# Kernel tuning notes

Hardware: AMD Instinct MI355X
Metric: run time of the kernel (lower is better)

Reference implementation:

```python
import jax, jax.numpy as jnp
import numpy as np


def _offdiag_cols(B):
    # cols[i, k] = k-th column index != i, ascending (matches masked_select on ~eye)
    r = jnp.arange(B - 1)[None, :]
    i = jnp.arange(B)[:, None]
    return jnp.where(r < i, r, r + 1)  # [B, B-1]


def _process_case(lan_s, vis, B):
    # lan_s: [B, D], vis: [B, V, D]
    lan_adj = lan_s @ lan_s.T                               # [B, B]
    # sim[b, a, v] = lan_s[b] . vis[a, v]  (torch 'avd,bqd->baqv' with q=1)
    sim = jnp.einsum('avd,bd->bav', vis, lan_s)             # [B, B, V]
    vals, idxs = jax.lax.top_k(sim, 2)                      # [B, B, 2]
    ar = jnp.arange(B)
    diag_idx = idxs[ar, ar, 0]                              # best region per matched pair
    selected = vis[ar, diag_idx]                            # [B, D]
    img_adj = selected @ selected.T                         # [B, B]
    # Slogits [B,B,1,1] -> max over trailing dims == plain matmul
    logits = selected @ lan_s.T                             # [B, B]

    max0 = vals[..., 0]                                     # [B, B]
    max1 = vals[..., 1]                                     # [B, B]
    cols = _offdiag_cols(B)
    max1_off = jnp.take_along_axis(max1, cols, axis=1)      # [B, B-1]
    new_logits = jnp.concatenate([max0, max1_off], axis=1)  # [B, 2B-1]
    # CrossEntropyLoss(mean) with target = arange(B)
    ce = -jnp.mean(jax.nn.log_softmax(new_logits, axis=1)[ar, ar])

    # Regularization pair loss on row-softmaxed max0; neg idx for sample i = all j != i,
    # duplicated (t2i and i2t are identical here) -> duplication cancels in the mean.
    score = jax.nn.softmax(max0, axis=1)                    # [B, B]
    d = jnp.diag(score)                                     # s_ii
    offmask = (1.0 - jnp.eye(B, dtype=score.dtype))
    denom = jnp.asarray(B * (B - 1), score.dtype)
    # t1[i,j] = |(s_ii - s_ji) - (s_jj - s_ij)|, t2[i,j] = |(s_ii - s_ij) - (s_jj - s_ji)|
    t1 = jnp.abs(d[:, None] - score.T - d[None, :] + score)
    t2 = jnp.abs(d[:, None] - score - d[None, :] + score.T)
    m1 = jnp.sum(t1 * offmask) / denom
    m2 = jnp.sum(t2 * offmask) / denom
    pairloss = jax.nn.relu(m1) + jax.nn.relu(m2)            # (L1 - margin).clamp(0), margin=0

    # L1 between adjacency softmax and logits softmax
    loss_fns = jnp.mean(jnp.abs(
        jax.nn.softmax((img_adj + lan_adj) * 0.5, axis=1) -
        jax.nn.softmax(logits, axis=1)))

    alpha = jnp.asarray(0.1, score.dtype)
    beta = jnp.asarray(0.1, score.dtype)
    return ce + alpha * loss_fns + beta * pairloss


def reference(vis_fs, lan_fs):
    B = vis_fs.shape[0]
    losses = [_process_case(lan_fs[:, i, :], vis_fs, B) for i in range(3)]
    return (losses[0] + losses[1] + losses[2]) / 3.0


def setup_inputs() -> dict:
    key = jax.random.key(0)
    k1, k2 = jax.random.split(key)
    B, V, D = 128, 784, 512
    # scale ~0.05 so dot products of D=512-dim embeddings stay in a sane softmax range
    vis_fs = jax.random.normal(k1, (B, V, D), dtype=jnp.float32) * 0.05
    lan_fs = jax.random.normal(k2, (B, 3, D), dtype=jnp.float32) * 0.05
    return {"vis_fs": vis_fs, "lan_fs": lan_fs}
```

## Files before the change

### kernel.cpp

```cpp
#include <hip/hip_runtime.h>
#include <math.h>

#define B_   128
#define V_   784
#define D_   512
#define M_   384
#define NCH  7
#define LO_OFF 196608

typedef __attribute__((ext_vector_type(8))) short short8;
typedef __attribute__((ext_vector_type(4))) float f32x4;

__device__ __forceinline__ ushort f2bf(float x) {
  uint u = __float_as_uint(x);
  u += 0x7fff + ((u >> 16) & 1);
  return (ushort)(u >> 16);
}
__device__ __forceinline__ float bf2f(ushort h) {
  return __uint_as_float((uint)h << 16);
}

__device__ __forceinline__ int swz(int row, int col) {
  return (row * 64 + col) ^ ((row & 7) << 3);
}

__device__ __forceinline__ short8 ldfrag(const ushort* base, int row, int col) {
  union { uint4 u; short8 s; } t;
  t.u = *(const uint4*)(base + swz(row, col));
  return t.s;
}

__global__ __launch_bounds__(256)
void prep_lan(const float* __restrict__ lan, ushort* __restrict__ lanbf,
              float* __restrict__ acc) {
  const int c = blockIdx.x, kb = blockIdx.y, t = threadIdx.x;
  if (c == 0 && kb == 0 && t < 12) acc[t] = 0.f;
  #pragma unroll
  for (int i = 0; i < 4; i++) {
    const int u = t + 256 * i;
    const int kk = u >> 9;
    const int m16 = (u >> 6) & 7;
    const int lane = u & 63;
    const int row = m16 * 16 + (lane & 15);
    const int k0 = kb * 64 + kk * 32 + (lane >> 4) * 8;
    const float4 v0 = *(const float4*)(lan + (size_t)(row * 3 + c) * D_ + k0);
    const float4 v1 = *(const float4*)(lan + (size_t)(row * 3 + c) * D_ + k0 + 4);
    union { ushort s[8]; uint4 u4; } h, l;
    const float vv[8] = {v0.x, v0.y, v0.z, v0.w, v1.x, v1.y, v1.z, v1.w};
    #pragma unroll
    for (int e = 0; e < 8; e++) {
      h.s[e] = f2bf(vv[e]);
      l.s[e] = f2bf(vv[e] - bf2f(h.s[e]));
    }
    const size_t ch = ((((size_t)(c * 8 + kb) * 2 + kk) * 8 + m16) * 64 + lane);
    *(uint4*)&lanbf[ch * 8] = h.u4;
    *(uint4*)&lanbf[LO_OFF + ch * 8] = l.u4;
  }
}

__global__ __launch_bounds__(512)
void gemm_top2(const float* __restrict__ vis, const ushort* __restrict__ lanbf,
               float* __restrict__ pv1, float* __restrict__ pv2,
               int* __restrict__ pi1) {
  const int id = blockIdx.x;
  const int a = id / NCH;
  const int nch = id - NCH * a;

  const int t = threadIdx.x;
  const int lane = t & 63, wid = t >> 6;
  const int tx = lane & 15, qq = lane >> 4;
  const int wr = wid >> 2, wc = wid & 3;

  __shared__ __align__(16) ushort Bsm[2][16384];

  f32x4 acc[3][4][2];
  const f32x4 zz = {0.f, 0.f, 0.f, 0.f};
  #pragma unroll
  for (int c = 0; c < 3; c++)
    #pragma unroll
    for (int m = 0; m < 4; m++)
      #pragma unroll
      for (int n = 0; n < 2; n++) acc[c][m][n] = zz;

  const int v0 = nch * 128;
  const float* visA = vis + (size_t)a * V_ * D_;

  float4 breg[4];
  #pragma unroll
  for (int i = 0; i < 4; i++) {
    const int f = t + 512 * i;
    const int row = f >> 4, col = (f & 15) * 4;
    const int vrow = v0 + row;
    breg[i] = (vrow < V_)
        ? *(const float4*)(visA + (size_t)vrow * D_ + col)
        : make_float4(0.f, 0.f, 0.f, 0.f);
  }
  #pragma unroll
  for (int i = 0; i < 4; i++) {
    const int f = t + 512 * i;
    const int row = f >> 4, col = (f & 15) * 4;
    const float4 v = breg[i];
    ushort4 h, l;
    h.x = f2bf(v.x); l.x = f2bf(v.x - bf2f(h.x));
    h.y = f2bf(v.y); l.y = f2bf(v.y - bf2f(h.y));
    h.z = f2bf(v.z); l.z = f2bf(v.z - bf2f(h.z));
    h.w = f2bf(v.w); l.w = f2bf(v.w - bf2f(h.w));
    const int e = swz(row, col);
    *(ushort4*)&Bsm[0][e] = h;
    *(ushort4*)&Bsm[0][8192 + e] = l;
  }
  __syncthreads();

  for (int kb = 0; kb < 8; kb++) {
    const int cur = kb & 1;
    if (kb < 7) {
      #pragma unroll
      for (int i = 0; i < 4; i++) {
        const int f = t + 512 * i;
        const int row = f >> 4, col = (f & 15) * 4;
        const int vrow = v0 + row;
        breg[i] = (vrow < V_)
            ? *(const float4*)(visA + (size_t)vrow * D_ + (kb + 1) * 64 + col)
            : make_float4(0.f, 0.f, 0.f, 0.f);
      }
    }
    const ushort* Bcur = &Bsm[cur][0];
    #pragma unroll
    for (int kk = 0; kk < 2; kk++) {
      short8 bh[2], bl[2];
      #pragma unroll
      for (int n = 0; n < 2; n++) {
        const int brow = 32 * wc + 16 * n + tx;
        const int bcol = kk * 32 + qq * 8;
        bh[n] = ldfrag(Bcur, brow, bcol);
        bl[n] = ldfrag(Bcur + 8192, brow, bcol);
      }
      #pragma unroll
      for (int c = 0; c < 3; c++) {
        const size_t ch0 =
            (((size_t)(c * 8 + kb) * 2 + kk) * 8 + wr * 4) * 64 + lane;
        short8 ah[4], al[4];
        #pragma unroll
        for (int m = 0; m < 4; m++) {
          ah[m] = *(const short8*)(lanbf + (ch0 + m * 64) * 8);
          al[m] = *(const short8*)(lanbf + (size_t)LO_OFF + (ch0 + m * 64) * 8);
        }
        #pragma unroll
        for (int m = 0; m < 4; m++)
          #pragma unroll
          for (int n = 0; n < 2; n++) {
            acc[c][m][n] = __builtin_amdgcn_mfma_f32_16x16x32_bf16(
                ah[m], bh[n], acc[c][m][n], 0, 0, 0);
            acc[c][m][n] = __builtin_amdgcn_mfma_f32_16x16x32_bf16(
                ah[m], bl[n], acc[c][m][n], 0, 0, 0);
            acc[c][m][n] = __builtin_amdgcn_mfma_f32_16x16x32_bf16(
                al[m], bh[n], acc[c][m][n], 0, 0, 0);
          }
      }
    }
    if (kb < 7) {
      #pragma unroll
      for (int i = 0; i < 4; i++) {
        const int f = t + 512 * i;
        const int row = f >> 4, col = (f & 15) * 4;
        const float4 v = breg[i];
        ushort4 h, l;
        h.x = f2bf(v.x); l.x = f2bf(v.x - bf2f(h.x));
        h.y = f2bf(v.y); l.y = f2bf(v.y - bf2f(h.y));
        h.z = f2bf(v.z); l.z = f2bf(v.z - bf2f(h.z));
        h.w = f2bf(v.w); l.w = f2bf(v.w - bf2f(h.w));
        const int e = swz(row, col);
        *(ushort4*)&Bsm[cur ^ 1][e] = h;
        *(ushort4*)&Bsm[cur ^ 1][8192 + e] = l;
      }
    }
    __syncthreads();
  }

  float* p1b = (float*)&Bsm[0][0];
  float* p2b = p1b + 512;
  int*   i1b = (int*)(p2b + 512);
  #pragma unroll
  for (int c = 0; c < 3; c++) {
    #pragma unroll
    for (int m = 0; m < 4; m++)
      #pragma unroll
      for (int r = 0; r < 4; r++) {
        float v1 = -INFINITY, v2 = -INFINITY;
        int i1 = 0x7fffffff;
        #pragma unroll
        for (int n = 0; n < 2; n++) {
          const int vv = v0 + 32 * wc + 16 * n + tx;
          const float x = acc[c][m][n][r];
          if (vv < V_) {
            if (x > v1) { v2 = v1; v1 = x; i1 = vv; }
            else if (x > v2) { v2 = x; }
          }
        }
        #pragma unroll
        for (int off = 8; off >= 1; off >>= 1) {
          const float ov1 = __shfl_xor(v1, off, 16);
          const float ov2 = __shfl_xor(v2, off, 16);
          const int   oi1 = __shfl_xor(i1, off, 16);
          if (ov1 > v1 || (ov1 == v1 && oi1 < i1)) {
            v2 = fmaxf(v1, ov2); v1 = ov1; i1 = oi1;
          } else {
            v2 = fmaxf(v2, ov1);
          }
        }
        if (tx == 0) {
          const int grow = 64 * wr + 16 * m + 4 * qq + r;
          p1b[wc * 128 + grow] = v1;
          p2b[wc * 128 + grow] = v2;
          i1b[wc * 128 + grow] = i1;
        }
      }
    __syncthreads();
    if (t < 128) {
      float v1 = p1b[t], v2 = p2b[t];
      int i1 = i1b[t];
      #pragma unroll
      for (int w = 1; w < 4; w++) {
        const float ov1 = p1b[w * 128 + t], ov2 = p2b[w * 128 + t];
        const int oi1 = i1b[w * 128 + t];
        if (ov1 > v1) { v2 = fmaxf(v1, ov2); v1 = ov1; i1 = oi1; }
        else          { v2 = fmaxf(v2, ov1); }
      }
      const size_t o = ((size_t)a * NCH + nch) * M_ + c * B_ + t;
      pv1[o] = v1; pv2[o] = v2; pi1[o] = i1;
    }
    __syncthreads();
  }
}

__global__ void reduce_top2(const float* __restrict__ pv1,
                            const float* __restrict__ pv2,
                            const int* __restrict__ pi1,
                            float* __restrict__ max0, float* __restrict__ max1,
                            int* __restrict__ didx) {
  const int idx = blockIdx.x * 256 + threadIdx.x;
  if (idx >= M_ * B_) return;
  const int m = idx >> 7, a = idx & 127;
  float v1 = -INFINITY, v2 = -INFINITY;
  int i1 = 0x7fffffff;
  #pragma unroll
  for (int nc = 0; nc < NCH; nc++) {
    const size_t o = ((size_t)a * NCH + nc) * M_ + m;
    const float ov1 = pv1[o], ov2 = pv2[o];
    const int oi1 = pi1[o];
    if (ov1 > v1 || (ov1 == v1 && oi1 < i1)) {
      v2 = fmaxf(v1, ov2); v1 = ov1; i1 = oi1;
    } else {
      v2 = fmaxf(v2, ov1);
    }
  }
  max0[idx] = v1;
  max1[idx] = v2;
  const int b = m & 127, cc = m >> 7;
  if (b == a) didx[(cc << 7) + b] = i1;
}

__global__ void gather_sel(const float* __restrict__ vis,
                           const int* __restrict__ didx,
                           float* __restrict__ sel) {
  const int cb = blockIdx.x;
  const int b = cb & 127;
  const int v = didx[cb];
  const float4* src = (const float4*)(vis + ((size_t)b * V_ + v) * D_);
  float4* dst = (float4*)(sel + (size_t)cb * D_);
  dst[threadIdx.x] = src[threadIdx.x];
}

__global__ __launch_bounds__(256)
void small_gemms(const float* __restrict__ lan, const float* __restrict__ sel,
                 float* __restrict__ lan_adj, float* __restrict__ img_adj,
                 float* __restrict__ logits) {
  const int c = blockIdx.z, g = blockIdx.y;
  const int t = threadIdx.x;
  const int j = t & 127;
  const int i0 = blockIdx.x * 8 + (t >> 7) * 4;
  const float4* xp[4];
  const float4* yp;
  float* O;
  #pragma unroll
  for (int r = 0; r < 4; r++) {
    const int i = i0 + r;
    xp[r] = (g == 0) ? (const float4*)(lan + (size_t)(i * 3 + c) * D_)
                     : (const float4*)(sel + ((size_t)c * B_ + i) * D_);
  }
  if (g == 1) yp = (const float4*)(sel + ((size_t)c * B_ + j) * D_);
  else yp = (const float4*)(lan + (size_t)(j * 3 + c) * D_);
  O = (g == 0) ? lan_adj : (g == 1) ? img_adj : logits;

  float s[4] = {0.f, 0.f, 0.f, 0.f};
  #pragma unroll 4
  for (int k = 0; k < D_ / 4; k++) {
    const float4 y = yp[k];
    #pragma unroll
    for (int r = 0; r < 4; r++) {
      const float4 x = xp[r][k];
      s[r] += x.x * y.x + x.y * y.y + x.z * y.z + x.w * y.w;
    }
  }
  #pragma unroll
  for (int r = 0; r < 4; r++)
    O[(size_t)c * (B_ * B_) + (size_t)(i0 + r) * B_ + j] = s[r];
}

__device__ __forceinline__ float wsum(float v) {
  #pragma unroll
  for (int m = 32; m >= 1; m >>= 1) v += __shfl_xor(v, m);
  return v;
}
__device__ __forceinline__ float wmax(float v) {
  #pragma unroll
  for (int m = 32; m >= 1; m >>= 1) v = fmaxf(v, __shfl_xor(v, m));
  return v;
}
__device__ __forceinline__ float bsum(float v, float* sb) {
  v = wsum(v);
  __syncthreads();
  if ((threadIdx.x & 63) == 0) sb[threadIdx.x >> 6] = v;
  __syncthreads();
  return sb[0] + sb[1];
}
__device__ __forceinline__ float bmax(float v, float* sb) {
  v = wmax(v);
  __syncthreads();
  if ((threadIdx.x & 63) == 0) sb[threadIdx.x >> 6] = v;
  __syncthreads();
  return fmaxf(sb[0], sb[1]);
}

__global__ __launch_bounds__(128)
void row_losses(const float* __restrict__ max0, const float* __restrict__ max1,
                const float* __restrict__ lan_adj, const float* __restrict__ img_adj,
                const float* __restrict__ logits, float* __restrict__ score,
                float* __restrict__ acc) {
  __shared__ float sb[2];
  const int c = blockIdx.y, i = blockIdx.x, j = threadIdx.x;
  const size_t row = ((size_t)c * B_ + i) * B_;
  const float m0 = max0[row + j];
  const float m1 = (j == i) ? -INFINITY : max1[row + j];

  const float rmax = bmax(fmaxf(m0, m1), sb);
  const float se = bsum(expf(m0 - rmax) + ((j == i) ? 0.f : expf(m1 - rmax)), sb);
  if (j == 0) {
    const float lse = logf(se) + rmax;
    atomicAdd(&acc[c], lse - max0[row + i]);
  }

  const float smax = bmax(m0, sb);
  const float e0 = expf(m0 - smax);
  const float ssum = bsum(e0, sb);
  score[row + j] = e0 / ssum;

  const float u = 0.5f * (lan_adj[row + j] + img_adj[row + j]);
  const float gg = logits[row + j];
  const float umax = bmax(u, sb);
  const float eu = expf(u - umax);
  const float usum = bsum(eu, sb);
  const float gmax = bmax(gg, sb);
  const float eg = expf(gg - gmax);
  const float gsum = bsum(eg, sb);
  const float dsum = bsum(fabsf(eu / usum - eg / gsum), sb);
  if (j == 0) atomicAdd(&acc[3 + c], dsum);
}

__global__ __launch_bounds__(256)
void pair_kernel(const float* __restrict__ score, float* __restrict__ acc) {
  const int c = blockIdx.y;
  const int idx = blockIdx.x * 256 + threadIdx.x;
  const int i = idx >> 7, j = idx & 127;
  const float* S = score + (size_t)c * (B_ * B_);
  float t1 = 0.f, t2 = 0.f;
  if (i != j) {
    const float dii = S[i * B_ + i], djj = S[j * B_ + j];
    const float sij = S[i * B_ + j], sji = S[j * B_ + i];
    t1 = fabsf(dii - sji - djj + sij);
    t2 = fabsf(dii - sij - djj + sji);
  }
  t1 = wsum(t1);
  t2 = wsum(t2);
  if ((threadIdx.x & 63) == 0) {
    atomicAdd(&acc[6 + c], t1);
    atomicAdd(&acc[9 + c], t2);
  }
}

__global__ void finalize(const float* __restrict__ acc, float* __restrict__ out) {
  if (threadIdx.x == 0 && blockIdx.x == 0) {
    float total = 0.f;
    const float denom = (float)(B_ * (B_ - 1));
    for (int c = 0; c < 3; c++) {
      const float ce  = acc[c] / (float)B_;
      const float fns = acc[3 + c] / (float)(B_ * B_);
      const float p1  = acc[6 + c] / denom;
      const float p2  = acc[9 + c] / denom;
      total += ce + 0.1f * fns + 0.1f * (fmaxf(p1, 0.f) + fmaxf(p2, 0.f));
    }
    out[0] = total / 3.f;
  }
}

extern "C" void kernel_launch(void* const* d_in, const int* in_sizes, int n_in,
                              void* d_out, int out_size, void* d_ws, size_t ws_size,
                              hipStream_t stream) {
  const float* vis = (const float*)d_in[0];
  const float* lan = (const float*)d_in[1];
  float* out = (float*)d_out;

  float* w = (float*)d_ws;
  float* pv1 = w;
  float* pv2 = pv1 + (size_t)M_ * B_ * NCH;
  int*   pi1 = (int*)(pv2 + (size_t)M_ * B_ * NCH);
  float* max0 = (float*)(pi1 + (size_t)M_ * B_ * NCH);
  float* max1 = max0 + 3 * B_ * B_;
  int*   didx = (int*)(max1 + 3 * B_ * B_);
  float* sel = (float*)(didx + 3 * B_);
  float* lan_adj = sel + (size_t)3 * B_ * D_;
  float* img_adj = lan_adj + 3 * B_ * B_;
  float* logits  = img_adj + 3 * B_ * B_;
  float* score   = logits + 3 * B_ * B_;
  float* acc     = score + 3 * B_ * B_;
  ushort* lanbf  = (ushort*)(acc + 16);

  prep_lan<<<dim3(3, 8), dim3(256), 0, stream>>>(lan, lanbf, acc);
  gemm_top2<<<dim3(B_ * NCH), dim3(512), 0, stream>>>(vis, lanbf, pv1, pv2, pi1);
  reduce_top2<<<dim3((M_ * B_ + 255) / 256), dim3(256), 0, stream>>>(
      pv1, pv2, pi1, max0, max1, didx);
  gather_sel<<<dim3(3 * B_), dim3(128), 0, stream>>>(vis, didx, sel);
  small_gemms<<<dim3(16, 3, 3), dim3(256), 0, stream>>>(
      lan, sel, lan_adj, img_adj, logits);
  row_losses<<<dim3(B_, 3), dim3(128), 0, stream>>>(
      max0, max1, lan_adj, img_adj, logits, score, acc);
  pair_kernel<<<dim3(B_ * B_ / 256, 3), dim3(256), 0, stream>>>(score, acc);
  finalize<<<dim3(1), dim3(1), 0, stream>>>(acc, out);
}
```

Before: 599.3 us.

## Stage GEMM operands via direct global-to-LDS loads and fuse tail kernels

The main GEMM now stages both the pre-split lan bf16 tiles and the raw fp32 vis tiles into LDS with global_load_lds (16 stages of K=32, double-buffered, 128KB LDS). The bf16 hi/lo split of vis now happens at fragment-read time, and the warp tiling changes to 4x2. The small GEMMs are fused into the row-loss kernel, and the pair and finalize kernels are merged into one block, cutting launches and intermediate buffers. The intent is to remove register staging, conversion stores and kernel launch overhead. The cost is a large LDS footprint per block and a single-block tail kernel.

Result: faster. 532.1 us (-11.2%).

```diff
diff --git a/kernel.cpp b/kernel.cpp
--- a/kernel.cpp
+++ b/kernel.cpp
@@ -6,10 +6,10 @@
 #define D_   512
 #define M_   384
 #define NCH  7
-#define LO_OFF 196608
 
 typedef __attribute__((ext_vector_type(8))) short short8;
 typedef __attribute__((ext_vector_type(4))) float f32x4;
+typedef unsigned int u32t;
 
 __device__ __forceinline__ ushort f2bf(float x) {
   uint u = __float_as_uint(x);
@@ -20,177 +20,156 @@
   return __uint_as_float((uint)h << 16);
 }
 
-__device__ __forceinline__ int swz(int row, int col) {
-  return (row * 64 + col) ^ ((row & 7) << 3);
-}
-
-__device__ __forceinline__ short8 ldfrag(const ushort* base, int row, int col) {
-  union { uint4 u; short8 s; } t;
-  t.u = *(const uint4*)(base + swz(row, col));
-  return t.s;
+__device__ __forceinline__ void stage16(const void* g, void* l) {
+  __builtin_amdgcn_global_load_lds(
+      (const __attribute__((address_space(1))) u32t*)g,
+      (__attribute__((address_space(3))) u32t*)(uintptr_t)l, 16, 0, 0);
 }
 
 __global__ __launch_bounds__(256)
 void prep_lan(const float* __restrict__ lan, ushort* __restrict__ lanbf,
               float* __restrict__ acc) {
-  const int c = blockIdx.x, kb = blockIdx.y, t = threadIdx.x;
-  if (c == 0 && kb == 0 && t < 12) acc[t] = 0.f;
-  #pragma unroll
-  for (int i = 0; i < 4; i++) {
-    const int u = t + 256 * i;
-    const int kk = u >> 9;
-    const int m16 = (u >> 6) & 7;
-    const int lane = u & 63;
+  const int c = blockIdx.x >> 4, s = blockIdx.x & 15, t = threadIdx.x;
+  if (blockIdx.x == 0 && t < 12) acc[t] = 0.f;
+  #pragma unroll
+  for (int it = 0; it < 2; ++it) {
+    const int u = t + it * 256;
+    const int m16 = u >> 6, lane = u & 63;
     const int row = m16 * 16 + (lane & 15);
-    const int k0 = kb * 64 + kk * 32 + (lane >> 4) * 8;
-    const float4 v0 = *(const float4*)(lan + (size_t)(row * 3 + c) * D_ + k0);
-    const float4 v1 = *(const float4*)(lan + (size_t)(row * 3 + c) * D_ + k0 + 4);
-    union { ushort s[8]; uint4 u4; } h, l;
-    const float vv[8] = {v0.x, v0.y, v0.z, v0.w, v1.x, v1.y, v1.z, v1.w};
-    #pragma unroll
-    for (int e = 0; e < 8; e++) {
-      h.s[e] = f2bf(vv[e]);
-      l.s[e] = f2bf(vv[e] - bf2f(h.s[e]));
-    }
-    const size_t ch = ((((size_t)(c * 8 + kb) * 2 + kk) * 8 + m16) * 64 + lane);
-    *(uint4*)&lanbf[ch * 8] = h.u4;
-    *(uint4*)&lanbf[LO_OFF + ch * 8] = l.u4;
-  }
-}
-
-__global__ __launch_bounds__(512)
+    const int k = s * 32 + (lane >> 4) * 8;
+    const float* src = lan + (size_t)(row * 3 + c) * D_ + k;
+    const float4 v0 = *(const float4*)src;
+    const float4 v1 = *(const float4*)(src + 4);
+    union { ushort s[8]; uint4 q; } H, L;
+    const float f[8] = {v0.x, v0.y, v0.z, v0.w, v1.x, v1.y, v1.z, v1.w};
+    #pragma unroll
+    for (int e = 0; e < 8; ++e) {
+      const ushort h = f2bf(f[e]);
+      H.s[e] = h; L.s[e] = f2bf(f[e] - bf2f(h));
+    }
+    const size_t base = ((size_t)(c * 16 + s) * 2) * 8 * 512;
+    *(uint4*)&lanbf[base + (size_t)m16 * 512 + lane * 8] = H.q;
+    *(uint4*)&lanbf[base + 4096 + (size_t)m16 * 512 + lane * 8] = L.q;
+  }
+}
+
+__global__ __launch_bounds__(512, 2)
 void gemm_top2(const float* __restrict__ vis, const ushort* __restrict__ lanbf,
                float* __restrict__ pv1, float* __restrict__ pv2,
                int* __restrict__ pi1) {
+  __shared__ __align__(16) char Lds[131072];
+
   const int id = blockIdx.x;
   const int a = id / NCH;
   const int nch = id - NCH * a;
-
   const int t = threadIdx.x;
   const int lane = t & 63, wid = t >> 6;
   const int tx = lane & 15, qq = lane >> 4;
-  const int wr = wid >> 2, wc = wid & 3;
-
-  __shared__ __align__(16) ushort Bsm[2][16384];
-
-  f32x4 acc[3][4][2];
+  const int wr = wid >> 1, wc = wid & 1;
+  const int v0 = nch * 128;
+  const char* visA = (const char*)vis + (size_t)a * V_ * D_ * 4;
+
+  const char* gb[8];
+  int gstep[8], ldso[8];
+  #pragma unroll
+  for (int gq = 0; gq < 8; ++gq) {
+    const int I = wid * 8 + gq;
+    ldso[gq] = I * 1024;
+    if (I < 48) {
+      const int c = I >> 4, sub = I & 15;
+      gb[gq] = (const char*)lanbf + (size_t)c * 262144 + sub * 1024 + lane * 16;
+      gstep[gq] = 16384;
+    } else {
+      const int v16 = (I - 48) >> 1, hb = (I - 48) & 1;
+      const int vp = (lane >> 1) & 15;
+      const int q2 = hb * 2 + (lane >> 5);
+      const int f4 = lane & 1;
+      int v = v0 + v16 * 16 + vp;
+      if (v > V_ - 1) v = V_ - 1;
+      gb[gq] = visA + (size_t)v * 2048 + q2 * 32 + f4 * 16;
+      gstep[gq] = 128;
+    }
+  }
+
+  f32x4 acc[3][2][4];
   const f32x4 zz = {0.f, 0.f, 0.f, 0.f};
   #pragma unroll
-  for (int c = 0; c < 3; c++)
-    #pragma unroll
-    for (int m = 0; m < 4; m++)
-      #pragma unroll
-      for (int n = 0; n < 2; n++) acc[c][m][n] = zz;
-
-  const int v0 = nch * 128;
-  const float* visA = vis + (size_t)a * V_ * D_;
-
-  float4 breg[4];
-  #pragma unroll
-  for (int i = 0; i < 4; i++) {
-    const int f = t + 512 * i;
-    const int row = f >> 4, col = (f & 15) * 4;
-    const int vrow = v0 + row;
-    breg[i] = (vrow < V_)
-        ? *(const float4*)(visA + (size_t)vrow * D_ + col)
-        : make_float4(0.f, 0.f, 0.f, 0.f);
-  }
-  #pragma unroll
-  for (int i = 0; i < 4; i++) {
-    const int f = t + 512 * i;
-    const int row = f >> 4, col = (f & 15) * 4;
-    const float4 v = breg[i];
-    ushort4 h, l;
-    h.x = f2bf(v.x); l.x = f2bf(v.x - bf2f(h.x));
-    h.y = f2bf(v.y); l.y = f2bf(v.y - bf2f(h.y));
-    h.z = f2bf(v.z); l.z = f2bf(v.z - bf2f(h.z));
-    h.w = f2bf(v.w); l.w = f2bf(v.w - bf2f(h.w));
-    const int e = swz(row, col);
-    *(ushort4*)&Bsm[0][e] = h;
-    *(ushort4*)&Bsm[0][8192 + e] = l;
-  }
-  __syncthreads();
-
-  for (int kb = 0; kb < 8; kb++) {
-    const int cur = kb & 1;
-    if (kb < 7) {
-      #pragma unroll
-      for (int i = 0; i < 4; i++) {
-        const int f = t + 512 * i;
-        const int row = f >> 4, col = (f & 15) * 4;
-        const int vrow = v0 + row;
-        breg[i] = (vrow < V_)
-            ? *(const float4*)(visA + (size_t)vrow * D_ + (kb + 1) * 64 + col)
-            : make_float4(0.f, 0.f, 0.f, 0.f);
+  for (int c = 0; c < 3; ++c)
+    #pragma unroll
+    for (int m = 0; m < 2; ++m)
+      #pragma unroll
+      for (int n = 0; n < 4; ++n) acc[c][m][n] = zz;
+
+  #pragma unroll
+  for (int gq = 0; gq < 8; ++gq) stage16(gb[gq], Lds + ldso[gq]);
+  asm volatile("s_waitcnt vmcnt(0)" ::: "memory");
+  __builtin_amdgcn_s_barrier();
+  asm volatile("" ::: "memory");
+
+  for (int s = 0; s < 16; ++s) {
+    const int buf = s & 1;
+    char* Lb = Lds + buf * 65536;
+    if (s < 15) {
+      char* Ln = Lds + (buf ^ 1) * 65536;
+      #pragma unroll
+      for (int gq = 0; gq < 8; ++gq)
+        stage16(gb[gq] + (size_t)(s + 1) * gstep[gq], Ln + ldso[gq]);
+    }
+    short8 bh[4], bl[4];
+    #pragma unroll
+    for (int n = 0; n < 4; ++n) {
+      const char* bp = Lb + 49152 + (wc * 4 + n) * 2048 + lane * 32;
+      const float4 x = *(const float4*)bp;
+      const float4 y = *(const float4*)(bp + 16);
+      union { ushort s[8]; short8 v; } H, L;
+      const float f[8] = {x.x, x.y, x.z, x.w, y.x, y.y, y.z, y.w};
+      #pragma unroll
+      for (int e = 0; e < 8; ++e) {
+        const ushort h = f2bf(f[e]);
+        H.s[e] = h; L.s[e] = f2bf(f[e] - bf2f(h));
       }
-    }
-    const ushort* Bcur = &Bsm[cur][0];
-    #pragma unroll
-    for (int kk = 0; kk < 2; kk++) {
-      short8 bh[2], bl[2];
-      #pragma unroll
-      for (int n = 0; n < 2; n++) {
-        const int brow = 32 * wc + 16 * n + tx;
-        const int bcol = kk * 32 + qq * 8;
-        bh[n] = ldfrag(Bcur, brow, bcol);
-        bl[n] = ldfrag(Bcur + 8192, brow, bcol);
+      bh[n] = H.v; bl[n] = L.v;
+    }
+    #pragma unroll
+    for (int c = 0; c < 3; ++c) {
+      short8 ah[2], al[2];
+      #pragma unroll
+      for (int m = 0; m < 2; ++m) {
+        const int sub = wr * 2 + m;
+        ah[m] = *(const short8*)(Lb + (c * 16 + sub) * 1024 + lane * 16);
+        al[m] = *(const short8*)(Lb + (c * 16 + 8 + sub) * 1024 + lane * 16);
       }
       #pragma unroll
-      for (int c = 0; c < 3; c++) {
-        const size_t ch0 =
-            (((size_t)(c * 8 + kb) * 2 + kk) * 8 + wr * 4) * 64 + lane;
-        short8 ah[4], al[4];
+      for (int m = 0; m < 2; ++m)
         #pragma unroll
-        for (int m = 0; m < 4; m++) {
-          ah[m] = *(const short8*)(lanbf + (ch0 + m * 64) * 8);
-          al[m] = *(const short8*)(lanbf + (size_t)LO_OFF + (ch0 + m * 64) * 8);
+        for (int n = 0; n < 4; ++n) {
+          acc[c][m][n] = __builtin_amdgcn_mfma_f32_16x16x32_bf16(
+              ah[m], bh[n], acc[c][m][n], 0, 0, 0);
+          acc[c][m][n] = __builtin_amdgcn_mfma_f32_16x16x32_bf16(
+              ah[m], bl[n], acc[c][m][n], 0, 0, 0);
+          acc[c][m][n] = __builtin_amdgcn_mfma_f32_16x16x32_bf16(
+              al[m], bh[n], acc[c][m][n], 0, 0, 0);
         }
-        #pragma unroll
-        for (int m = 0; m < 4; m++)
-          #pragma unroll
-          for (int n = 0; n < 2; n++) {
-            acc[c][m][n] = __builtin_amdgcn_mfma_f32_16x16x32_bf16(
-                ah[m], bh[n], acc[c][m][n], 0, 0, 0);
-            acc[c][m][n] = __builtin_amdgcn_mfma_f32_16x16x32_bf16(
-                ah[m], bl[n], acc[c][m][n], 0, 0, 0);
-            acc[c][m][n] = __builtin_amdgcn_mfma_f32_16x16x32_bf16(
-                al[m], bh[n], acc[c][m][n], 0, 0, 0);
-          }
-      }
-    }
-    if (kb < 7) {
-      #pragma unroll
-      for (int i = 0; i < 4; i++) {
-        const int f = t + 512 * i;
-        const int row = f >> 4, col = (f & 15) * 4;
-        const float4 v = breg[i];
-        ushort4 h, l;
-        h.x = f2bf(v.x); l.x = f2bf(v.x - bf2f(h.x));
-        h.y = f2bf(v.y); l.y = f2bf(v.y - bf2f(h.y));
-        h.z = f2bf(v.z); l.z = f2bf(v.z - bf2f(h.z));
-        h.w = f2bf(v.w); l.w = f2bf(v.w - bf2f(h.w));
-        const int e = swz(row, col);
-        *(ushort4*)&Bsm[cur ^ 1][e] = h;
-        *(ushort4*)&Bsm[cur ^ 1][8192 + e] = l;
-      }
-    }
-    __syncthreads();
-  }
-
-  float* p1b = (float*)&Bsm[0][0];
-  float* p2b = p1b + 512;
-  int*   i1b = (int*)(p2b + 512);
-  #pragma unroll
-  for (int c = 0; c < 3; c++) {
-    #pragma unroll
-    for (int m = 0; m < 4; m++)
-      #pragma unroll
-      for (int r = 0; r < 4; r++) {
+    }
+    if (s < 15) asm volatile("s_waitcnt vmcnt(0)" ::: "memory");
+    __builtin_amdgcn_s_barrier();
+    asm volatile("" ::: "memory");
+  }
+
+  float* p1b = (float*)Lds;
+  float* p2b = p1b + 256;
+  int*   i1b = (int*)(p2b + 256);
+  #pragma unroll
+  for (int c = 0; c < 3; ++c) {
+    #pragma unroll
+    for (int m = 0; m < 2; ++m)
+      #pragma unroll
+      for (int r = 0; r < 4; ++r) {
         float v1 = -INFINITY, v2 = -INFINITY;
         int i1 = 0x7fffffff;
         #pragma unroll
-        for (int n = 0; n < 2; n++) {
-          const int vv = v0 + 32 * wc + 16 * n + tx;
+        for (int n = 0; n < 4; ++n) {
+          const int vv = v0 + wc * 64 + n * 16 + tx;
           const float x = acc[c][m][n][r];
           if (vv < V_) {
             if (x > v1) { v2 = v1; v1 = x; i1 = vv; }
@@ -209,7 +188,7 @@
           }
         }
         if (tx == 0) {
-          const int grow = 64 * wr + 16 * m + 4 * qq + r;
+          const int grow = wr * 32 + m * 16 + qq * 4 + r;
           p1b[wc * 128 + grow] = v1;
           p2b[wc * 128 + grow] = v2;
           i1b[wc * 128 + grow] = i1;
@@ -219,13 +198,10 @@
     if (t < 128) {
       float v1 = p1b[t], v2 = p2b[t];
       int i1 = i1b[t];
-      #pragma unroll
-      for (int w = 1; w < 4; w++) {
-        const float ov1 = p1b[w * 128 + t], ov2 = p2b[w * 128 + t];
-        const int oi1 = i1b[w * 128 + t];
-        if (ov1 > v1) { v2 = fmaxf(v1, ov2); v1 = ov1; i1 = oi1; }
-        else          { v2 = fmaxf(v2, ov1); }
-      }
+      const float ov1 = p1b[128 + t], ov2 = p2b[128 + t];
+      const int oi1 = i1b[128 + t];
+      if (ov1 > v1) { v2 = fmaxf(v1, ov2); v1 = ov1; i1 = oi1; }
+      else          { v2 = fmaxf(v2, ov1); }
       const size_t o = ((size_t)a * NCH + nch) * M_ + c * B_ + t;
       pv1[o] = v1; pv2[o] = v2; pi1[o] = i1;
     }
@@ -271,136 +247,133 @@
   dst[threadIdx.x] = src[threadIdx.x];
 }
 
-__global__ __launch_bounds__(256)
-void small_gemms(const float* __restrict__ lan, const float* __restrict__ sel,
-                 float* __restrict__ lan_adj, float* __restrict__ img_adj,
-                 float* __restrict__ logits) {
-  const int c = blockIdx.z, g = blockIdx.y;
-  const int t = threadIdx.x;
-  const int j = t & 127;
-  const int i0 = blockIdx.x * 8 + (t >> 7) * 4;
-  const float4* xp[4];
-  const float4* yp;
-  float* O;
-  #pragma unroll
-  for (int r = 0; r < 4; r++) {
-    const int i = i0 + r;
-    xp[r] = (g == 0) ? (const float4*)(lan + (size_t)(i * 3 + c) * D_)
-                     : (const float4*)(sel + ((size_t)c * B_ + i) * D_);
-  }
-  if (g == 1) yp = (const float4*)(sel + ((size_t)c * B_ + j) * D_);
-  else yp = (const float4*)(lan + (size_t)(j * 3 + c) * D_);
-  O = (g == 0) ? lan_adj : (g == 1) ? img_adj : logits;
-
-  float s[4] = {0.f, 0.f, 0.f, 0.f};
-  #pragma unroll 4
-  for (int k = 0; k < D_ / 4; k++) {
-    const float4 y = yp[k];
-    #pragma unroll
-    for (int r = 0; r < 4; r++) {
-      const float4 x = xp[r][k];
-      s[r] += x.x * y.x + x.y * y.y + x.z * y.z + x.w * y.w;
-    }
-  }
-  #pragma unroll
-  for (int r = 0; r < 4; r++)
-    O[(size_t)c * (B_ * B_) + (size_t)(i0 + r) * B_ + j] = s[r];
-}
-
-__device__ __forceinline__ float wsum(float v) {
+__device__ __forceinline__ float wsum64(float v) {
   #pragma unroll
   for (int m = 32; m >= 1; m >>= 1) v += __shfl_xor(v, m);
   return v;
 }
-__device__ __forceinline__ float wmax(float v) {
+__device__ __forceinline__ float wmax64(float v) {
   #pragma unroll
   for (int m = 32; m >= 1; m >>= 1) v = fmaxf(v, __shfl_xor(v, m));
   return v;
 }
-__device__ __forceinline__ float bsum(float v, float* sb) {
-  v = wsum(v);
+__device__ __forceinline__ float halfsum(float v, float* sb, int rr, int t) {
+  v = wsum64(v);
   __syncthreads();
-  if ((threadIdx.x & 63) == 0) sb[threadIdx.x >> 6] = v;
+  if ((t & 63) == 0) sb[t >> 6] = v;
   __syncthreads();
-  return sb[0] + sb[1];
-}
-__device__ __forceinline__ float bmax(float v, float* sb) {
-  v = wmax(v);
+  return sb[rr * 2] + sb[rr * 2 + 1];
+}
+__device__ __forceinline__ float halfmax(float v, float* sb, int rr, int t) {
+  v = wmax64(v);
   __syncthreads();
-  if ((threadIdx.x & 63) == 0) sb[threadIdx.x >> 6] = v;
+  if ((t & 63) == 0) sb[t >> 6] = v;
   __syncthreads();
-  return fmaxf(sb[0], sb[1]);
-}
-
-__global__ __launch_bounds__(128)
-void row_losses(const float* __restrict__ max0, const float* __restrict__ max1,
-                const float* __restrict__ lan_adj, const float* __restrict__ img_adj,
-                const float* __restrict__ logits, float* __restrict__ score,
-                float* __restrict__ acc) {
-  __shared__ float sb[2];
-  const int c = blockIdx.y, i = blockIdx.x, j = threadIdx.x;
+  return fmaxf(sb[rr * 2], sb[rr * 2 + 1]);
+}
+
+__global__ __launch_bounds__(256)
+void adj_losses(const float* __restrict__ lan, const float* __restrict__ sel,
+                const float* __restrict__ max0, const float* __restrict__ max1,
+                float* __restrict__ score, float* __restrict__ acc) {
+  __shared__ float sb[4];
+  __shared__ float sdiag[2];
+  const int c = blockIdx.y;
+  const int t = threadIdx.x;
+  const int rr = t >> 7, j = t & 127;
+  const int i = blockIdx.x * 2 + rr;
+
+  const float4* xl = (const float4*)(lan + (size_t)(i * 3 + c) * D_);
+  const float4* xs = (const float4*)(sel + ((size_t)c * B_ + i) * D_);
+  const float4* yl = (const float4*)(lan + (size_t)(j * 3 + c) * D_);
+  const float4* ys = (const float4*)(sel + ((size_t)c * B_ + j) * D_);
+  float sll = 0.f, sss = 0.f, ssl = 0.f;
+  #pragma unroll 4
+  for (int k = 0; k < D_ / 4; ++k) {
+    const float4 A = xl[k], Bv = yl[k], C = xs[k], Dv = ys[k];
+    sll += A.x * Bv.x + A.y * Bv.y + A.z * Bv.z + A.w * Bv.w;
+    sss += C.x * Dv.x + C.y * Dv.y + C.z * Dv.z + C.w * Dv.w;
+    ssl += C.x * Bv.x + C.y * Bv.y + C.z * Bv.z + C.w * Bv.w;
+  }
+  const float u = 0.5f * (sll + sss);
+  const float g = ssl;
+
   const size_t row = ((size_t)c * B_ + i) * B_;
   const float m0 = max0[row + j];
   const float m1 = (j == i) ? -INFINITY : max1[row + j];
-
-  const float rmax = bmax(fmaxf(m0, m1), sb);
-  const float se = bsum(expf(m0 - rmax) + ((j == i) ? 0.f : expf(m1 - rmax)), sb);
-  if (j == 0) {
-    const float lse = logf(se) + rmax;
-    atomicAdd(&acc[c], lse - max0[row + i]);
-  }
-
-  const float smax = bmax(m0, sb);
+  if (j == i) sdiag[rr] = m0;
+
+  const float rmax = halfmax(fmaxf(m0, m1), sb, rr, t);
+  const float se =
+      halfsum(expf(m0 - rmax) + ((j == i) ? 0.f : expf(m1 - rmax)), sb, rr, t);
+  if (j == 0) atomicAdd(&acc[c], logf(se) + rmax - sdiag[rr]);
+
+  const float smax = halfmax(m0, sb, rr, t);
   const float e0 = expf(m0 - smax);
-  const float ssum = bsum(e0, sb);
+  const float ssum = halfsum(e0, sb, rr, t);
   score[row + j] = e0 / ssum;
 
-  const float u = 0.5f * (lan_adj[row + j] + img_adj[row + j]);
-  const float gg = logits[row + j];
-  const float umax = bmax(u, sb);
+  const float umax = halfmax(u, sb, rr, t);
   const float eu = expf(u - umax);
-  const float usum = bsum(eu, sb);
-  const float gmax = bmax(gg, sb);
-  const float eg = expf(gg - gmax);
-  const float gsum = bsum(eg, sb);
-  const float dsum = bsum(fabsf(eu / usum - eg / gsum), sb);
+  const float usum = halfsum(eu, sb, rr, t);
+  const float gmax = halfmax(g, sb, rr, t);
+  const float eg = expf(g - gmax);
+  const float gsum = halfsum(eg, sb, rr, t);
+  const float dsum = halfsum(fabsf(eu / usum - eg / gsum), sb, rr, t);
   if (j == 0) atomicAdd(&acc[3 + c], dsum);
 }
 
-__global__ __launch_bounds__(256)
-void pair_kernel(const float* __restrict__ score, float* __restrict__ acc) {
-  const int c = blockIdx.y;
-  const int idx = blockIdx.x * 256 + threadIdx.x;
-  const int i = idx >> 7, j = idx & 127;
-  const float* S = score + (size_t)c * (B_ * B_);
-  float t1 = 0.f, t2 = 0.f;
-  if (i != j) {
-    const float dii = S[i * B_ + i], djj = S[j * B_ + j];
-    const float sij = S[i * B_ + j], sji = S[j * B_ + i];
-    t1 = fabsf(dii - sji - djj + sij);
-    t2 = fabsf(dii - sij - djj + sji);
-  }
-  t1 = wsum(t1);
-  t2 = wsum(t2);
-  if ((threadIdx.x & 63) == 0) {
-    atomicAdd(&acc[6 + c], t1);
-    atomicAdd(&acc[9 + c], t2);
-  }
-}
-
-__global__ void finalize(const float* __restrict__ acc, float* __restrict__ out) {
-  if (threadIdx.x == 0 && blockIdx.x == 0) {
-    float total = 0.f;
-    const float denom = (float)(B_ * (B_ - 1));
-    for (int c = 0; c < 3; c++) {
-      const float ce  = acc[c] / (float)B_;
+__global__ __launch_bounds__(1024)
+void pair_finalize(const float* __restrict__ score, const float* __restrict__ acc,
+                   float* __restrict__ out) {
+  __shared__ float diag[M_];
+  __shared__ float sb[16];
+  const int t = threadIdx.x;
+  if (t < M_) diag[t] = score[(size_t)t * 128 + (t & 127)];
+  __syncthreads();
+
+  float gtot = 0.f;
+  #pragma unroll
+  for (int c = 0; c < 3; ++c) {
+    float t1 = 0.f, t2 = 0.f;
+    const float* S = score + (size_t)c * (B_ * B_);
+    const float* Dg = diag + c * B_;
+    #pragma unroll
+    for (int it = 0; it < 16; ++it) {
+      const int ij = it * 1024 + t;
+      const int i = ij >> 7, j = ij & 127;
+      if (i != j) {
+        const float sij = S[i * B_ + j], sji = S[j * B_ + i];
+        const float dii = Dg[i], djj = Dg[j];
+        t1 += fabsf(dii - sji - djj + sij);
+        t2 += fabsf(dii - sij - djj + sji);
+      }
+    }
+    t1 = wsum64(t1);
+    t2 = wsum64(t2);
+    __syncthreads();
+    if ((t & 63) == 0) sb[t >> 6] = t1;
+    __syncthreads();
+    float r1 = 0.f, r2 = 0.f;
+    if (t == 0) {
+      #pragma unroll
+      for (int w = 0; w < 16; ++w) r1 += sb[w];
+    }
+    __syncthreads();
+    if ((t & 63) == 0) sb[t >> 6] = t2;
+    __syncthreads();
+    if (t == 0) {
+      #pragma unroll
+      for (int w = 0; w < 16; ++w) r2 += sb[w];
+      const float den = (float)(B_ * (B_ - 1));
+      const float ce = acc[c] / (float)B_;
       const float fns = acc[3 + c] / (float)(B_ * B_);
-      const float p1  = acc[6 + c] / denom;
-      const float p2  = acc[9 + c] / denom;
-      total += ce + 0.1f * fns + 0.1f * (fmaxf(p1, 0.f) + fmaxf(p2, 0.f));
-    }
-    out[0] = total / 3.f;
-  }
+      gtot += ce + 0.1f * fns +
+              0.1f * (fmaxf(r1 / den, 0.f) + fmaxf(r2 / den, 0.f));
+    }
+    __syncthreads();
+  }
+  if (t == 0) out[0] = gtot / 3.f;
 }
 
 extern "C" void kernel_launch(void* const* d_in, const int* in_sizes, int n_in,
@@ -417,23 +390,17 @@
   float* max0 = (float*)(pi1 + (size_t)M_ * B_ * NCH);
   float* max1 = max0 + 3 * B_ * B_;
   int*   didx = (int*)(max1 + 3 * B_ * B_);
-  float* sel = (float*)(didx + 3 * B_);
-  float* lan_adj = sel + (size_t)3 * B_ * D_;
-  float* img_adj = lan_adj + 3 * B_ * B_;
-  float* logits  = img_adj + 3 * B_ * B_;
-  float* score   = logits + 3 * B_ * B_;
-  float* acc     = score + 3 * B_ * B_;
-  ushort* lanbf  = (ushort*)(acc + 16);
-
-  prep_lan<<<dim3(3, 8), dim3(256), 0, stream>>>(lan, lanbf, acc);
+  float* sel  = (float*)(didx + 3 * B_);
+  float* score = sel + (size_t)3 * B_ * D_;
+  float* acc   = score + 3 * B_ * B_;
+  ushort* lanbf = (ushort*)(acc + 16);
+
+  prep_lan<<<dim3(48), dim3(256), 0, stream>>>(lan, lanbf, acc);
   gemm_top2<<<dim3(B_ * NCH), dim3(512), 0, stream>>>(vis, lanbf, pv1, pv2, pi1);
   reduce_top2<<<dim3((M_ * B_ + 255) / 256), dim3(256), 0, stream>>>(
       pv1, pv2, pi1, max0, max1, didx);
   gather_sel<<<dim3(3 * B_), dim3(128), 0, stream>>>(vis, didx, sel);
-  small_gemms<<<dim3(16, 3, 3), dim3(256), 0, stream>>>(
-      lan, sel, lan_adj, img_adj, logits);
-  row_losses<<<dim3(B_, 3), dim3(128), 0, stream>>>(
-      max0, max1, lan_adj, img_adj, logits, score, acc);
-  pair_kernel<<<dim3(B_ * B_ / 256, 3), dim3(256), 0, stream>>>(score, acc);
-  finalize<<<dim3(1), dim3(1), 0, stream>>>(acc, out);
-}
+  adj_losses<<<dim3(B_ / 2, 3), dim3(256), 0, stream>>>(
+      lan, sel, max0, max1, score, acc);
+  pair_finalize<<<dim3(1), dim3(1024), 0, stream>>>(score, acc, out);
+}
```
